# Kernel optimization log

Measured on AMD Instinct MI355X. Metric: run time of the kernel, lower is better.

The kernel has to match this reference:

```python
import jax, jax.numpy as jnp
import numpy as np

MARGIN = 0.3
NEG_FILL = 1e9  # larger than any real distance; keeps min-reduction valid


def setup_inputs() -> dict:
    key = jax.random.key(0)
    k1, k2 = jax.random.split(key)
    embeddings = jax.random.normal(k1, (4096, 256), dtype=jnp.float32)
    labels = jax.random.randint(k2, (4096,), 0, 512, dtype=jnp.int64)
    return {"embeddings": embeddings, "labels": labels}


def _pairwise_distances(embeddings):
    # Faithful to the torch version, including the zero-distance sqrt guard.
    dot = jnp.matmul(embeddings, embeddings.T)          # [B, B]
    sq = jnp.diagonal(dot)                              # [B]
    d2 = sq[None, :] - 2.0 * dot + sq[:, None]
    d2 = jnp.maximum(d2, 0.0)
    zero_mask = (d2 == 0.0).astype(embeddings.dtype)
    d = jnp.sqrt(d2 + zero_mask * 1e-16)
    return d * (1.0 - zero_mask)


def reference(embeddings, labels):
    B = labels.shape[0]
    d = _pairwise_distances(embeddings)                 # [B, B]

    same = labels[:, None] == labels[None, :]           # [B, B]
    eye = jnp.eye(B, dtype=bool)
    pos_mask = same & ~eye
    neg_mask = ~same

    has_pos = jnp.any(pos_mask, axis=1)
    has_neg = jnp.any(neg_mask, axis=1)
    valid = has_pos & has_neg                           # [B]

    # Row-wise masked reductions (distances >= 0 so -1 is a safe max fill).
    hardest_pos = jnp.max(jnp.where(pos_mask, d, -1.0), axis=1)
    hardest_neg = jnp.min(jnp.where(neg_mask, d, NEG_FILL), axis=1)

    per_anchor = jnp.maximum(hardest_pos - hardest_neg + MARGIN, 0.0)
    n_valid = jnp.sum(valid.astype(jnp.float32))
    total = jnp.sum(jnp.where(valid, per_anchor, 0.0))
    return jnp.where(n_valid > 0, total / jnp.maximum(n_valid, 1.0), 0.0)
```

## Files before the change

kernel.cpp:

```cpp
#include <hip/hip_runtime.h>
#include <hip/hip_fp16.h>

#define BN 4096
#define DIM 256
#define NBLK 32
#define NPAIR 528
#define MARGIN_F 0.3f
#define NEG_FILL_F 1e9f
#define HP_SENT_BITS 0xBF800000

typedef __attribute__((ext_vector_type(8))) _Float16 f16x8;
typedef __attribute__((ext_vector_type(4))) float f32x4;

__device__ __forceinline__ void gld_lds16(const void* g, void* l) {
    __builtin_amdgcn_global_load_lds(
        (const __attribute__((address_space(1))) unsigned int*)g,
        (__attribute__((address_space(3))) unsigned int*)l, 16, 0, 0);
}

__global__ __launch_bounds__(256) void tl_prep(const float* __restrict__ E,
                                               float* __restrict__ norms,
                                               float* __restrict__ red,
                                               ushort* __restrict__ Eh) {
    const int tid  = threadIdx.x;
    const int lane = tid & 63;
    const int row  = blockIdx.x * 4 + (tid >> 6);

    float4 v = reinterpret_cast<const float4*>(E + (size_t)row * DIM)[lane];
    float f[4] = {v.x, v.y, v.z, v.w};
    ushort hb[4];
    float s = 0.0f;
    #pragma unroll
    for (int q = 0; q < 4; ++q) {
        s += f[q] * f[q];
        hb[q] = __half_as_ushort(__float2half(f[q]));
    }
    const int kc = lane >> 1, half = lane & 1;
    const size_t co = (((size_t)(kc * BN + row)) << 3) + (size_t)(half * 4);
    *reinterpret_cast<ushort4*>(Eh + co) = make_ushort4(hb[0], hb[1], hb[2], hb[3]);

    #pragma unroll
    for (int m = 32; m; m >>= 1) s += __shfl_xor(s, m, 64);
    if (lane == 0) norms[row] = s;
    if (blockIdx.x == 0 && tid < 3) red[tid] = 0.0f;
}

__global__ __launch_bounds__(256) void tl_main(const ushort* __restrict__ Eh,
                                               const int* __restrict__ labels,
                                               const float* __restrict__ norms,
                                               float* __restrict__ pHP,
                                               float* __restrict__ pHN) {
    __shared__ __align__(16) ushort smem[2][16384];

    const int tid  = threadIdx.x;
    const int lane = tid & 63;
    const int wave = tid >> 6;
    const int wy = wave >> 1, wx = wave & 1;
    const int quad = lane >> 4, l15 = lane & 15;

    int t = blockIdx.x, ib = 0, off = 0;
    while (off + (NBLK - ib) <= t) { off += NBLK - ib; ++ib; }
    const int jb = ib + (t - off);
    const int i0 = ib * 128, j0 = jb * 128;

    f32x4 acc[4][4];
    #pragma unroll
    for (int r = 0; r < 4; ++r)
        #pragma unroll
        for (int c = 0; c < 4; ++c)
            acc[r][c] = (f32x4){0.f, 0.f, 0.f, 0.f};

    auto stage = [&](int kb, int buf) {
        #pragma unroll
        for (int s = 0; s < 8; ++s) {
            const int idx  = s * 256 + tid;
            const int part = idx >> 10;
            const int kc   = (idx >> 7) & 7;
            const int m    = idx & 127;
            const int base = part ? j0 : i0;
            const ushort* src = Eh + (((size_t)((kb * 8 + kc) * BN + base + m)) << 3);
            gld_lds16(src, &smem[buf][idx << 3]);
        }
    };

    stage(0, 0);
    #pragma unroll
    for (int kb = 0; kb < DIM / 64; ++kb) {
        const int buf = kb & 1;
        __syncthreads();
        if (kb + 1 < DIM / 64) stage(kb + 1, buf ^ 1);

        const ushort* sb = &smem[buf][0];
        #pragma unroll
        for (int h = 0; h < 2; ++h) {
            f16x8 a[4], b[4];
            #pragma unroll
            for (int r = 0; r < 4; ++r) {
                const int mi = wy * 64 + r * 16 + l15;
                a[r] = *reinterpret_cast<const f16x8*>(&sb[(((h * 4 + quad) * 128) + mi) * 8]);
            }
            #pragma unroll
            for (int c = 0; c < 4; ++c) {
                const int ni = wx * 64 + c * 16 + l15;
                b[c] = *reinterpret_cast<const f16x8*>(&sb[((1024 + (h * 4 + quad) * 128) + ni) * 8]);
            }
            #pragma unroll
            for (int c = 0; c < 4; ++c)
                #pragma unroll
                for (int r = 0; r < 4; ++r)
                    acc[r][c] = __builtin_amdgcn_mfma_f32_16x16x32_f16(a[r], b[c], acc[r][c], 0, 0, 0);
        }
    }

    const int rowBase = i0 + wy * 64;
    const int colBase = j0 + wx * 64;

    float nrow[4][4]; int lrow[4][4];
    #pragma unroll
    for (int r = 0; r < 4; ++r)
        #pragma unroll
        for (int e = 0; e < 4; ++e) {
            const int g = rowBase + r * 16 + quad * 4 + e;
            nrow[r][e] = norms[g];
            lrow[r][e] = labels[g];
        }
    float ncol[4]; int lcol[4];
    #pragma unroll
    for (int c = 0; c < 4; ++c) {
        const int g = colBase + c * 16 + l15;
        ncol[c] = norms[g];
        lcol[c] = labels[g];
    }

    float rmax[4][4], rmin[4][4], cmax[4], cmin[4];
    #pragma unroll
    for (int r = 0; r < 4; ++r)
        #pragma unroll
        for (int e = 0; e < 4; ++e) { rmax[r][e] = -1.0f; rmin[r][e] = NEG_FILL_F; }
    #pragma unroll
    for (int c = 0; c < 4; ++c) { cmax[c] = -1.0f; cmin[c] = NEG_FILL_F; }

    #pragma unroll
    for (int c = 0; c < 4; ++c) {
        const int gcol = colBase + c * 16 + l15;
        #pragma unroll
        for (int r = 0; r < 4; ++r) {
            #pragma unroll
            for (int e = 0; e < 4; ++e) {
                const int grow = rowBase + r * 16 + quad * 4 + e;
                float d2 = nrow[r][e] + ncol[c] - 2.0f * acc[r][c][e];
                d2 = fmaxf(d2, 0.0f);
                const float d = (d2 > 0.0f) ? sqrtf(d2) : 0.0f;
                if (lrow[r][e] == lcol[c]) {
                    if (grow != gcol) {
                        rmax[r][e] = fmaxf(rmax[r][e], d);
                        cmax[c]    = fmaxf(cmax[c], d);
                    }
                } else {
                    rmin[r][e] = fminf(rmin[r][e], d);
                    cmin[c]    = fminf(cmin[c], d);
                }
            }
        }
    }

    #pragma unroll
    for (int m = 1; m <= 8; m <<= 1) {
        #pragma unroll
        for (int r = 0; r < 4; ++r)
            #pragma unroll
            for (int e = 0; e < 4; ++e) {
                rmax[r][e] = fmaxf(rmax[r][e], __shfl_xor(rmax[r][e], m, 64));
                rmin[r][e] = fminf(rmin[r][e], __shfl_xor(rmin[r][e], m, 64));
            }
    }
    #pragma unroll
    for (int m = 16; m <= 32; m <<= 1) {
        #pragma unroll
        for (int c = 0; c < 4; ++c) {
            cmax[c] = fmaxf(cmax[c], __shfl_xor(cmax[c], m, 64));
            cmin[c] = fminf(cmin[c], __shfl_xor(cmin[c], m, 64));
        }
    }

    int*      srhp = reinterpret_cast<int*>(&smem[0][0]);
    unsigned* srhn = reinterpret_cast<unsigned*>(srhp + 128);
    int*      schp = srhp + 256;
    unsigned* schn = reinterpret_cast<unsigned*>(srhp + 384);
    __syncthreads();
    if (tid < 128) {
        srhp[tid] = (int)HP_SENT_BITS;
        srhn[tid] = __float_as_uint(NEG_FILL_F);
        schp[tid] = (int)HP_SENT_BITS;
        schn[tid] = __float_as_uint(NEG_FILL_F);
    }
    __syncthreads();
    if (l15 == 0) {
        #pragma unroll
        for (int r = 0; r < 4; ++r)
            #pragma unroll
            for (int e = 0; e < 4; ++e) {
                const int lr = wy * 64 + r * 16 + quad * 4 + e;
                atomicMax(&srhp[lr], __float_as_int(rmax[r][e]));
                atomicMin(&srhn[lr], __float_as_uint(rmin[r][e]));
            }
    }
    if (quad == 0) {
        #pragma unroll
        for (int c = 0; c < 4; ++c) {
            const int lc = wx * 64 + c * 16 + l15;
            atomicMax(&schp[lc], __float_as_int(cmax[c]));
            atomicMin(&schn[lc], __float_as_uint(cmin[c]));
        }
    }
    __syncthreads();
    if (tid < 128) {
        float rp = __int_as_float(srhp[tid]);
        float rn = __uint_as_float(srhn[tid]);
        const float cp = __int_as_float(schp[tid]);
        const float cn = __uint_as_float(schn[tid]);
        if (ib == jb) {
            pHP[(size_t)jb * BN + i0 + tid] = fmaxf(rp, cp);
            pHN[(size_t)jb * BN + i0 + tid] = fminf(rn, cn);
        } else {
            pHP[(size_t)jb * BN + i0 + tid] = rp;
            pHN[(size_t)jb * BN + i0 + tid] = rn;
            pHP[(size_t)ib * BN + j0 + tid] = cp;
            pHN[(size_t)ib * BN + j0 + tid] = cn;
        }
    }
}

__global__ __launch_bounds__(256) void tl_reduce(const float* __restrict__ pHP,
                                                 const float* __restrict__ pHN,
                                                 float* __restrict__ red,
                                                 float* __restrict__ out) {
    const int i = blockIdx.x * 256 + threadIdx.x;
    float hp = -1.0f, hn = NEG_FILL_F;
    #pragma unroll
    for (int s = 0; s < NBLK; ++s) {
        hp = fmaxf(hp, pHP[(size_t)s * BN + i]);
        hn = fminf(hn, pHN[(size_t)s * BN + i]);
    }
    const bool valid = (hp >= 0.0f) && (hn < NEG_FILL_F);
    const float per = fmaxf(hp - hn + MARGIN_F, 0.0f);
    float s_ = valid ? per : 0.0f;
    float c_ = valid ? 1.0f : 0.0f;
    #pragma unroll
    for (int m = 32; m; m >>= 1) {
        s_ += __shfl_xor(s_, m, 64);
        c_ += __shfl_xor(c_, m, 64);
    }
    __shared__ float as_[4], ac_[4];
    const int wid = threadIdx.x >> 6;
    if ((threadIdx.x & 63) == 0) { as_[wid] = s_; ac_[wid] = c_; }
    __syncthreads();
    if (threadIdx.x == 0) {
        const float S = as_[0] + as_[1] + as_[2] + as_[3];
        const float C = ac_[0] + ac_[1] + ac_[2] + ac_[3];
        atomicAdd(&red[0], S);
        atomicAdd(&red[1], C);
        __threadfence();
        const unsigned ticket = atomicAdd(reinterpret_cast<unsigned*>(&red[2]), 1u);
        if (ticket == gridDim.x - 1) {
            const float S2 = atomicAdd(&red[0], 0.0f);
            const float C2 = atomicAdd(&red[1], 0.0f);
            out[0] = (C2 > 0.0f) ? (S2 / fmaxf(C2, 1.0f)) : 0.0f;
        }
    }
}

extern "C" void kernel_launch(void* const* d_in, const int* in_sizes, int n_in,
                              void* d_out, int out_size, void* d_ws, size_t ws_size,
                              hipStream_t stream) {
    const float* E      = (const float*)d_in[0];
    const int*   labels = (const int*)d_in[1];

    float*  ws    = (float*)d_ws;
    float*  norms = ws;
    float*  red   = ws + 4096;
    float*  pHP   = ws + 8192;
    float*  pHN   = ws + 8192 + NBLK * BN;
    ushort* Eh    = (ushort*)(ws + 8192 + 2 * NBLK * BN);

    tl_prep<<<BN / 4, 256, 0, stream>>>(E, norms, red, Eh);
    tl_main<<<NPAIR, 256, 0, stream>>>(Eh, labels, norms, pHP, pHN);
    tl_reduce<<<BN / 256, 256, 0, stream>>>(pHP, pHN, red, (float*)d_out);
}
```

Before: 98.70 us.

## Split each tile pair into two half-column blocks and defer sqrt to reduce

Each 128x128 tile pair is now split into two 128x64 blocks, which doubles the grid to 1056 blocks and halves the B-operand staging and LDS footprint. Launch bounds request three blocks per CU. The per-element sqrt is removed: min and max are taken on squared distances and sqrt is applied only once per row in the reduce kernel. The cost is that A tiles are loaded twice, there are twice as many partial slots to write and reduce (64 instead of 32), and each block does less MFMA work.

```diff
diff --git a/kernel.cpp b/kernel.cpp
--- a/kernel.cpp
+++ b/kernel.cpp
@@ -5,6 +5,7 @@
 #define DIM 256
 #define NBLK 32
 #define NPAIR 528
+#define NSLOT 64
 #define MARGIN_F 0.3f
 #define NEG_FILL_F 1e9f
 #define HP_SENT_BITS 0xBF800000
@@ -45,12 +46,12 @@
     if (blockIdx.x == 0 && tid < 3) red[tid] = 0.0f;
 }
 
-__global__ __launch_bounds__(256) void tl_main(const ushort* __restrict__ Eh,
-                                               const int* __restrict__ labels,
-                                               const float* __restrict__ norms,
-                                               float* __restrict__ pHP,
-                                               float* __restrict__ pHN) {
-    __shared__ __align__(16) ushort smem[2][16384];
+__global__ __launch_bounds__(256, 3) void tl_main(const ushort* __restrict__ Eh,
+                                                  const int* __restrict__ labels,
+                                                  const float* __restrict__ norms,
+                                                  float* __restrict__ pHP,
+                                                  float* __restrict__ pHN) {
+    __shared__ __align__(16) ushort smem[2][12288];
 
     const int tid  = threadIdx.x;
     const int lane = tid & 63;
@@ -58,26 +59,28 @@
     const int wy = wave >> 1, wx = wave & 1;
     const int quad = lane >> 4, l15 = lane & 15;
 
-    int t = blockIdx.x, ib = 0, off = 0;
+    const int pair = blockIdx.x >> 1;
+    const int h    = blockIdx.x & 1;
+    int t = pair, ib = 0, off = 0;
     while (off + (NBLK - ib) <= t) { off += NBLK - ib; ++ib; }
     const int jb = ib + (t - off);
     const int i0 = ib * 128, j0 = jb * 128;
-
-    f32x4 acc[4][4];
+    const int j0c = j0 + h * 64;
+
+    f32x4 acc[4][2];
     #pragma unroll
     for (int r = 0; r < 4; ++r)
         #pragma unroll
-        for (int c = 0; c < 4; ++c)
+        for (int c = 0; c < 2; ++c)
             acc[r][c] = (f32x4){0.f, 0.f, 0.f, 0.f};
 
     auto stage = [&](int kb, int buf) {
         #pragma unroll
-        for (int s = 0; s < 8; ++s) {
-            const int idx  = s * 256 + tid;
-            const int part = idx >> 10;
-            const int kc   = (idx >> 7) & 7;
-            const int m    = idx & 127;
-            const int base = part ? j0 : i0;
+        for (int s = 0; s < 6; ++s) {
+            const int idx = s * 256 + tid;
+            int kc, m, base;
+            if (idx < 1024) { kc = idx >> 7; m = idx & 127; base = i0; }
+            else { const int r8 = idx - 1024; kc = r8 >> 6; m = r8 & 63; base = j0c; }
             const ushort* src = Eh + (((size_t)((kb * 8 + kc) * BN + base + m)) << 3);
             gld_lds16(src, &smem[buf][idx << 3]);
         }
@@ -92,20 +95,20 @@
 
         const ushort* sb = &smem[buf][0];
         #pragma unroll
-        for (int h = 0; h < 2; ++h) {
-            f16x8 a[4], b[4];
+        for (int h2 = 0; h2 < 2; ++h2) {
+            f16x8 a[4], b[2];
             #pragma unroll
             for (int r = 0; r < 4; ++r) {
                 const int mi = wy * 64 + r * 16 + l15;
-                a[r] = *reinterpret_cast<const f16x8*>(&sb[(((h * 4 + quad) * 128) + mi) * 8]);
-            }
-            #pragma unroll
-            for (int c = 0; c < 4; ++c) {
-                const int ni = wx * 64 + c * 16 + l15;
-                b[c] = *reinterpret_cast<const f16x8*>(&sb[((1024 + (h * 4 + quad) * 128) + ni) * 8]);
-            }
-            #pragma unroll
-            for (int c = 0; c < 4; ++c)
+                a[r] = *reinterpret_cast<const f16x8*>(&sb[(((h2 * 4 + quad) * 128) + mi) * 8]);
+            }
+            #pragma unroll
+            for (int c = 0; c < 2; ++c) {
+                const int ni = wx * 32 + c * 16 + l15;
+                b[c] = *reinterpret_cast<const f16x8*>(&sb[((1024 + (h2 * 4 + quad) * 64) + ni) * 8]);
+            }
+            #pragma unroll
+            for (int c = 0; c < 2; ++c)
                 #pragma unroll
                 for (int r = 0; r < 4; ++r)
                     acc[r][c] = __builtin_amdgcn_mfma_f32_16x16x32_f16(a[r], b[c], acc[r][c], 0, 0, 0);
@@ -113,7 +116,7 @@
     }
 
     const int rowBase = i0 + wy * 64;
-    const int colBase = j0 + wx * 64;
+    const int colBase = j0c + wx * 32;
 
     float nrow[4][4]; int lrow[4][4];
     #pragma unroll
@@ -124,41 +127,39 @@
             nrow[r][e] = norms[g];
             lrow[r][e] = labels[g];
         }
-    float ncol[4]; int lcol[4];
-    #pragma unroll
-    for (int c = 0; c < 4; ++c) {
+    float ncol[2]; int lcol[2];
+    #pragma unroll
+    for (int c = 0; c < 2; ++c) {
         const int g = colBase + c * 16 + l15;
         ncol[c] = norms[g];
         lcol[c] = labels[g];
     }
 
-    float rmax[4][4], rmin[4][4], cmax[4], cmin[4];
+    float rmax2[4][4], rmin2[4][4], cmax2[2], cmin2[2];
     #pragma unroll
     for (int r = 0; r < 4; ++r)
         #pragma unroll
-        for (int e = 0; e < 4; ++e) { rmax[r][e] = -1.0f; rmin[r][e] = NEG_FILL_F; }
-    #pragma unroll
-    for (int c = 0; c < 4; ++c) { cmax[c] = -1.0f; cmin[c] = NEG_FILL_F; }
-
-    #pragma unroll
-    for (int c = 0; c < 4; ++c) {
+        for (int e = 0; e < 4; ++e) { rmax2[r][e] = -1.0f; rmin2[r][e] = NEG_FILL_F; }
+    #pragma unroll
+    for (int c = 0; c < 2; ++c) { cmax2[c] = -1.0f; cmin2[c] = NEG_FILL_F; }
+
+    #pragma unroll
+    for (int c = 0; c < 2; ++c) {
         const int gcol = colBase + c * 16 + l15;
         #pragma unroll
         for (int r = 0; r < 4; ++r) {
             #pragma unroll
             for (int e = 0; e < 4; ++e) {
                 const int grow = rowBase + r * 16 + quad * 4 + e;
-                float d2 = nrow[r][e] + ncol[c] - 2.0f * acc[r][c][e];
-                d2 = fmaxf(d2, 0.0f);
-                const float d = (d2 > 0.0f) ? sqrtf(d2) : 0.0f;
+                float d2 = fmaxf(nrow[r][e] + ncol[c] - 2.0f * acc[r][c][e], 0.0f);
                 if (lrow[r][e] == lcol[c]) {
                     if (grow != gcol) {
-                        rmax[r][e] = fmaxf(rmax[r][e], d);
-                        cmax[c]    = fmaxf(cmax[c], d);
+                        rmax2[r][e] = fmaxf(rmax2[r][e], d2);
+                        cmax2[c]    = fmaxf(cmax2[c], d2);
                     }
                 } else {
-                    rmin[r][e] = fminf(rmin[r][e], d);
-                    cmin[c]    = fminf(cmin[c], d);
+                    rmin2[r][e] = fminf(rmin2[r][e], d2);
+                    cmin2[c]    = fminf(cmin2[c], d2);
                 }
             }
         }
@@ -170,27 +171,29 @@
         for (int r = 0; r < 4; ++r)
             #pragma unroll
             for (int e = 0; e < 4; ++e) {
-                rmax[r][e] = fmaxf(rmax[r][e], __shfl_xor(rmax[r][e], m, 64));
-                rmin[r][e] = fminf(rmin[r][e], __shfl_xor(rmin[r][e], m, 64));
+                rmax2[r][e] = fmaxf(rmax2[r][e], __shfl_xor(rmax2[r][e], m, 64));
+                rmin2[r][e] = fminf(rmin2[r][e], __shfl_xor(rmin2[r][e], m, 64));
             }
     }
     #pragma unroll
     for (int m = 16; m <= 32; m <<= 1) {
         #pragma unroll
-        for (int c = 0; c < 4; ++c) {
-            cmax[c] = fmaxf(cmax[c], __shfl_xor(cmax[c], m, 64));
-            cmin[c] = fminf(cmin[c], __shfl_xor(cmin[c], m, 64));
+        for (int c = 0; c < 2; ++c) {
+            cmax2[c] = fmaxf(cmax2[c], __shfl_xor(cmax2[c], m, 64));
+            cmin2[c] = fminf(cmin2[c], __shfl_xor(cmin2[c], m, 64));
         }
     }
 
     int*      srhp = reinterpret_cast<int*>(&smem[0][0]);
     unsigned* srhn = reinterpret_cast<unsigned*>(srhp + 128);
     int*      schp = srhp + 256;
-    unsigned* schn = reinterpret_cast<unsigned*>(srhp + 384);
+    unsigned* schn = reinterpret_cast<unsigned*>(srhp + 320);
     __syncthreads();
     if (tid < 128) {
         srhp[tid] = (int)HP_SENT_BITS;
         srhn[tid] = __float_as_uint(NEG_FILL_F);
+    }
+    if (tid < 64) {
         schp[tid] = (int)HP_SENT_BITS;
         schn[tid] = __float_as_uint(NEG_FILL_F);
     }
@@ -201,32 +204,33 @@
             #pragma unroll
             for (int e = 0; e < 4; ++e) {
                 const int lr = wy * 64 + r * 16 + quad * 4 + e;
-                atomicMax(&srhp[lr], __float_as_int(rmax[r][e]));
-                atomicMin(&srhn[lr], __float_as_uint(rmin[r][e]));
+                atomicMax(&srhp[lr], __float_as_int(rmax2[r][e]));
+                atomicMin(&srhn[lr], __float_as_uint(rmin2[r][e]));
             }
     }
     if (quad == 0) {
         #pragma unroll
-        for (int c = 0; c < 4; ++c) {
-            const int lc = wx * 64 + c * 16 + l15;
-            atomicMax(&schp[lc], __float_as_int(cmax[c]));
-            atomicMin(&schn[lc], __float_as_uint(cmin[c]));
+        for (int c = 0; c < 2; ++c) {
+            const int lc = wx * 32 + c * 16 + l15;
+            atomicMax(&schp[lc], __float_as_int(cmax2[c]));
+            atomicMin(&schn[lc], __float_as_uint(cmin2[c]));
         }
     }
     __syncthreads();
     if (tid < 128) {
-        float rp = __int_as_float(srhp[tid]);
-        float rn = __uint_as_float(srhn[tid]);
-        const float cp = __int_as_float(schp[tid]);
-        const float cn = __uint_as_float(schn[tid]);
+        const float rp = __int_as_float(srhp[tid]);
+        const float rn = __uint_as_float(srhn[tid]);
+        const bool  inh = ((tid >> 6) == h);
+        const float cp = inh ? __int_as_float(schp[tid & 63]) : -1.0f;
+        const float cn = inh ? __uint_as_float(schn[tid & 63]) : NEG_FILL_F;
         if (ib == jb) {
-            pHP[(size_t)jb * BN + i0 + tid] = fmaxf(rp, cp);
-            pHN[(size_t)jb * BN + i0 + tid] = fminf(rn, cn);
+            pHP[(size_t)(2 * ib + h) * BN + i0 + tid] = fmaxf(rp, cp);
+            pHN[(size_t)(2 * ib + h) * BN + i0 + tid] = fminf(rn, cn);
         } else {
-            pHP[(size_t)jb * BN + i0 + tid] = rp;
-            pHN[(size_t)jb * BN + i0 + tid] = rn;
-            pHP[(size_t)ib * BN + j0 + tid] = cp;
-            pHN[(size_t)ib * BN + j0 + tid] = cn;
+            pHP[(size_t)(2 * jb + h) * BN + i0 + tid] = rp;
+            pHN[(size_t)(2 * jb + h) * BN + i0 + tid] = rn;
+            pHP[(size_t)(2 * ib + h) * BN + j0 + tid] = cp;
+            pHN[(size_t)(2 * ib + h) * BN + j0 + tid] = cn;
         }
     }
 }
@@ -236,13 +240,15 @@
                                                  float* __restrict__ red,
                                                  float* __restrict__ out) {
     const int i = blockIdx.x * 256 + threadIdx.x;
-    float hp = -1.0f, hn = NEG_FILL_F;
-    #pragma unroll
-    for (int s = 0; s < NBLK; ++s) {
-        hp = fmaxf(hp, pHP[(size_t)s * BN + i]);
-        hn = fminf(hn, pHN[(size_t)s * BN + i]);
-    }
-    const bool valid = (hp >= 0.0f) && (hn < NEG_FILL_F);
+    float hp2 = -1.0f, hn2 = NEG_FILL_F;
+    #pragma unroll
+    for (int s = 0; s < NSLOT; ++s) {
+        hp2 = fmaxf(hp2, pHP[(size_t)s * BN + i]);
+        hn2 = fminf(hn2, pHN[(size_t)s * BN + i]);
+    }
+    const bool valid = (hp2 >= 0.0f) && (hn2 < NEG_FILL_F);
+    const float hp = sqrtf(fmaxf(hp2, 0.0f));
+    const float hn = sqrtf(hn2);
     const float per = fmaxf(hp - hn + MARGIN_F, 0.0f);
     float s_ = valid ? per : 0.0f;
     float c_ = valid ? 1.0f : 0.0f;
@@ -280,10 +286,10 @@
     float*  norms = ws;
     float*  red   = ws + 4096;
     float*  pHP   = ws + 8192;
-    float*  pHN   = ws + 8192 + NBLK * BN;
-    ushort* Eh    = (ushort*)(ws + 8192 + 2 * NBLK * BN);
+    float*  pHN   = ws + 8192 + NSLOT * BN;
+    ushort* Eh    = (ushort*)(ws + 8192 + 2 * NSLOT * BN);
 
     tl_prep<<<BN / 4, 256, 0, stream>>>(E, norms, red, Eh);
-    tl_main<<<NPAIR, 256, 0, stream>>>(Eh, labels, norms, pHP, pHN);
+    tl_main<<<NPAIR * 2, 256, 0, stream>>>(Eh, labels, norms, pHP, pHN);
     tl_reduce<<<BN / 256, 256, 0, stream>>>(pHP, pHN, red, (float*)d_out);
 }
```

Result: slower. 102.1 us (+3.4%).

## Reduce on squared distances and load full K tile into LDS at once

Applied to the files above, without the earlier changes.

The masked max/min reductions now run on squared distances, and the sqrt moves to the final per-anchor reduce kernel. Because sqrt is monotonic the selected extremes are the same, so roughly 16M sqrt calls in the epilogue drop to about 8K. The double-buffered K loop is also replaced by a single up-front load of the whole 256-deep tile into a 128 KB LDS buffer, followed by one barrier. This removes the per-stage syncs, but it loses the overlap between loading and MFMA work and raises LDS use per block, which can limit occupancy to one block per CU.

```diff
diff --git a/kernel.cpp b/kernel.cpp
--- a/kernel.cpp
+++ b/kernel.cpp
@@ -5,6 +5,7 @@
 #define DIM 256
 #define NBLK 32
 #define NPAIR 528
+#define NSLOT 32
 #define MARGIN_F 0.3f
 #define NEG_FILL_F 1e9f
 #define HP_SENT_BITS 0xBF800000
@@ -50,7 +51,7 @@
                                                const float* __restrict__ norms,
                                                float* __restrict__ pHP,
                                                float* __restrict__ pHN) {
-    __shared__ __align__(16) ushort smem[2][16384];
+    __shared__ __align__(16) ushort smem[65536];
 
     const int tid  = threadIdx.x;
     const int lane = tid & 63;
@@ -63,6 +64,18 @@
     const int jb = ib + (t - off);
     const int i0 = ib * 128, j0 = jb * 128;
 
+    #pragma unroll
+    for (int s = 0; s < 32; ++s) {
+        const int idx  = s * 256 + tid;
+        const int part = idx >> 12;
+        const int kc   = (idx >> 7) & 31;
+        const int m    = idx & 127;
+        const int base = part ? j0 : i0;
+        const ushort* src = Eh + (((size_t)(kc * BN + base + m)) << 3);
+        gld_lds16(src, &smem[idx << 3]);
+    }
+    __syncthreads();
+
     f32x4 acc[4][4];
     #pragma unroll
     for (int r = 0; r < 4; ++r)
@@ -70,46 +83,24 @@
         for (int c = 0; c < 4; ++c)
             acc[r][c] = (f32x4){0.f, 0.f, 0.f, 0.f};
 
-    auto stage = [&](int kb, int buf) {
-        #pragma unroll
-        for (int s = 0; s < 8; ++s) {
-            const int idx  = s * 256 + tid;
-            const int part = idx >> 10;
-            const int kc   = (idx >> 7) & 7;
-            const int m    = idx & 127;
-            const int base = part ? j0 : i0;
-            const ushort* src = Eh + (((size_t)((kb * 8 + kc) * BN + base + m)) << 3);
-            gld_lds16(src, &smem[buf][idx << 3]);
-        }
-    };
-
-    stage(0, 0);
-    #pragma unroll
-    for (int kb = 0; kb < DIM / 64; ++kb) {
-        const int buf = kb & 1;
-        __syncthreads();
-        if (kb + 1 < DIM / 64) stage(kb + 1, buf ^ 1);
-
-        const ushort* sb = &smem[buf][0];
-        #pragma unroll
-        for (int h = 0; h < 2; ++h) {
-            f16x8 a[4], b[4];
-            #pragma unroll
-            for (int r = 0; r < 4; ++r) {
-                const int mi = wy * 64 + r * 16 + l15;
-                a[r] = *reinterpret_cast<const f16x8*>(&sb[(((h * 4 + quad) * 128) + mi) * 8]);
-            }
-            #pragma unroll
-            for (int c = 0; c < 4; ++c) {
-                const int ni = wx * 64 + c * 16 + l15;
-                b[c] = *reinterpret_cast<const f16x8*>(&sb[((1024 + (h * 4 + quad) * 128) + ni) * 8]);
-            }
-            #pragma unroll
-            for (int c = 0; c < 4; ++c)
-                #pragma unroll
-                for (int r = 0; r < 4; ++r)
-                    acc[r][c] = __builtin_amdgcn_mfma_f32_16x16x32_f16(a[r], b[c], acc[r][c], 0, 0, 0);
-        }
+    #pragma unroll
+    for (int t8 = 0; t8 < 8; ++t8) {
+        f16x8 a[4], b[4];
+        #pragma unroll
+        for (int r = 0; r < 4; ++r) {
+            const int mi = wy * 64 + r * 16 + l15;
+            a[r] = *reinterpret_cast<const f16x8*>(&smem[(((t8 * 4 + quad) * 128) + mi) * 8]);
+        }
+        #pragma unroll
+        for (int c = 0; c < 4; ++c) {
+            const int ni = wx * 64 + c * 16 + l15;
+            b[c] = *reinterpret_cast<const f16x8*>(&smem[(32768 + ((t8 * 4 + quad) * 128 + ni) * 8)]);
+        }
+        #pragma unroll
+        for (int c = 0; c < 4; ++c)
+            #pragma unroll
+            for (int r = 0; r < 4; ++r)
+                acc[r][c] = __builtin_amdgcn_mfma_f32_16x16x32_f16(a[r], b[c], acc[r][c], 0, 0, 0);
     }
 
     const int rowBase = i0 + wy * 64;
@@ -132,13 +123,13 @@
         lcol[c] = labels[g];
     }
 
-    float rmax[4][4], rmin[4][4], cmax[4], cmin[4];
+    float rmax2[4][4], rmin2[4][4], cmax2[4], cmin2[4];
     #pragma unroll
     for (int r = 0; r < 4; ++r)
         #pragma unroll
-        for (int e = 0; e < 4; ++e) { rmax[r][e] = -1.0f; rmin[r][e] = NEG_FILL_F; }
-    #pragma unroll
-    for (int c = 0; c < 4; ++c) { cmax[c] = -1.0f; cmin[c] = NEG_FILL_F; }
+        for (int e = 0; e < 4; ++e) { rmax2[r][e] = -1.0f; rmin2[r][e] = NEG_FILL_F; }
+    #pragma unroll
+    for (int c = 0; c < 4; ++c) { cmax2[c] = -1.0f; cmin2[c] = NEG_FILL_F; }
 
     #pragma unroll
     for (int c = 0; c < 4; ++c) {
@@ -148,17 +139,15 @@
             #pragma unroll
             for (int e = 0; e < 4; ++e) {
                 const int grow = rowBase + r * 16 + quad * 4 + e;
-                float d2 = nrow[r][e] + ncol[c] - 2.0f * acc[r][c][e];
-                d2 = fmaxf(d2, 0.0f);
-                const float d = (d2 > 0.0f) ? sqrtf(d2) : 0.0f;
+                float d2 = fmaxf(nrow[r][e] + ncol[c] - 2.0f * acc[r][c][e], 0.0f);
                 if (lrow[r][e] == lcol[c]) {
                     if (grow != gcol) {
-                        rmax[r][e] = fmaxf(rmax[r][e], d);
-                        cmax[c]    = fmaxf(cmax[c], d);
+                        rmax2[r][e] = fmaxf(rmax2[r][e], d2);
+                        cmax2[c]    = fmaxf(cmax2[c], d2);
                     }
                 } else {
-                    rmin[r][e] = fminf(rmin[r][e], d);
-                    cmin[c]    = fminf(cmin[c], d);
+                    rmin2[r][e] = fminf(rmin2[r][e], d2);
+                    cmin2[c]    = fminf(cmin2[c], d2);
                 }
             }
         }
@@ -170,20 +159,20 @@
         for (int r = 0; r < 4; ++r)
             #pragma unroll
             for (int e = 0; e < 4; ++e) {
-                rmax[r][e] = fmaxf(rmax[r][e], __shfl_xor(rmax[r][e], m, 64));
-                rmin[r][e] = fminf(rmin[r][e], __shfl_xor(rmin[r][e], m, 64));
+                rmax2[r][e] = fmaxf(rmax2[r][e], __shfl_xor(rmax2[r][e], m, 64));
+                rmin2[r][e] = fminf(rmin2[r][e], __shfl_xor(rmin2[r][e], m, 64));
             }
     }
     #pragma unroll
     for (int m = 16; m <= 32; m <<= 1) {
         #pragma unroll
         for (int c = 0; c < 4; ++c) {
-            cmax[c] = fmaxf(cmax[c], __shfl_xor(cmax[c], m, 64));
-            cmin[c] = fminf(cmin[c], __shfl_xor(cmin[c], m, 64));
-        }
-    }
-
-    int*      srhp = reinterpret_cast<int*>(&smem[0][0]);
+            cmax2[c] = fmaxf(cmax2[c], __shfl_xor(cmax2[c], m, 64));
+            cmin2[c] = fminf(cmin2[c], __shfl_xor(cmin2[c], m, 64));
+        }
+    }
+
+    int*      srhp = reinterpret_cast<int*>(&smem[0]);
     unsigned* srhn = reinterpret_cast<unsigned*>(srhp + 128);
     int*      schp = srhp + 256;
     unsigned* schn = reinterpret_cast<unsigned*>(srhp + 384);
@@ -201,22 +190,22 @@
             #pragma unroll
             for (int e = 0; e < 4; ++e) {
                 const int lr = wy * 64 + r * 16 + quad * 4 + e;
-                atomicMax(&srhp[lr], __float_as_int(rmax[r][e]));
-                atomicMin(&srhn[lr], __float_as_uint(rmin[r][e]));
+                atomicMax(&srhp[lr], __float_as_int(rmax2[r][e]));
+                atomicMin(&srhn[lr], __float_as_uint(rmin2[r][e]));
             }
     }
     if (quad == 0) {
         #pragma unroll
         for (int c = 0; c < 4; ++c) {
             const int lc = wx * 64 + c * 16 + l15;
-            atomicMax(&schp[lc], __float_as_int(cmax[c]));
-            atomicMin(&schn[lc], __float_as_uint(cmin[c]));
+            atomicMax(&schp[lc], __float_as_int(cmax2[c]));
+            atomicMin(&schn[lc], __float_as_uint(cmin2[c]));
         }
     }
     __syncthreads();
     if (tid < 128) {
-        float rp = __int_as_float(srhp[tid]);
-        float rn = __uint_as_float(srhn[tid]);
+        const float rp = __int_as_float(srhp[tid]);
+        const float rn = __uint_as_float(srhn[tid]);
         const float cp = __int_as_float(schp[tid]);
         const float cn = __uint_as_float(schn[tid]);
         if (ib == jb) {
@@ -236,13 +225,15 @@
                                                  float* __restrict__ red,
                                                  float* __restrict__ out) {
     const int i = blockIdx.x * 256 + threadIdx.x;
-    float hp = -1.0f, hn = NEG_FILL_F;
-    #pragma unroll
-    for (int s = 0; s < NBLK; ++s) {
-        hp = fmaxf(hp, pHP[(size_t)s * BN + i]);
-        hn = fminf(hn, pHN[(size_t)s * BN + i]);
-    }
-    const bool valid = (hp >= 0.0f) && (hn < NEG_FILL_F);
+    float hp2 = -1.0f, hn2 = NEG_FILL_F;
+    #pragma unroll
+    for (int s = 0; s < NSLOT; ++s) {
+        hp2 = fmaxf(hp2, pHP[(size_t)s * BN + i]);
+        hn2 = fminf(hn2, pHN[(size_t)s * BN + i]);
+    }
+    const bool valid = (hp2 >= 0.0f) && (hn2 < NEG_FILL_F);
+    const float hp = sqrtf(fmaxf(hp2, 0.0f));
+    const float hn = sqrtf(hn2);
     const float per = fmaxf(hp - hn + MARGIN_F, 0.0f);
     float s_ = valid ? per : 0.0f;
     float c_ = valid ? 1.0f : 0.0f;
@@ -280,8 +271,8 @@
     float*  norms = ws;
     float*  red   = ws + 4096;
     float*  pHP   = ws + 8192;
-    float*  pHN   = ws + 8192 + NBLK * BN;
-    ushort* Eh    = (ushort*)(ws + 8192 + 2 * NBLK * BN);
+    float*  pHN   = ws + 8192 + NSLOT * BN;
+    ushort* Eh    = (ushort*)(ws + 8192 + 2 * NSLOT * BN);
 
     tl_prep<<<BN / 4, 256, 0, stream>>>(E, norms, red, Eh);
     tl_main<<<NPAIR, 256, 0, stream>>>(Eh, labels, norms, pHP, pHN);
```

New measurement: 98.95 us. Within noise of the previous version (+0.3%).
